# Kernel tuning notes

Measured on AMD Instinct MI355X. Metric: run time of the kernel, lower is better.

## Reference

```python
import jax, jax.numpy as jnp
import numpy as np

B, L = 128, 1024


def setup_inputs() -> dict:
    key = jax.random.key(0)
    k1, k2 = jax.random.split(key)
    y_pred = jax.random.normal(k1, (B, L), dtype=jnp.float32)
    y_true = jax.random.randint(k2, (B, L), 0, 2, dtype=jnp.int32)
    return {"y_pred": y_pred, "y_true": y_true}


def reference(y_pred, y_true):
    # pos/neg masks per row; original treats ==1 as pos, ==0 as neg
    pos = (y_true == 1)  # [B, L]
    neg = (y_true == 0)  # [B, L]
    # pairwise hinge: relu(1 - s_pos + s_neg) over all (pos, neg) pairs per row
    diff = 1.0 - y_pred[:, :, None] + y_pred[:, None, :]        # [B, L, L]
    pair_mask = pos[:, :, None] & neg[:, None, :]                # [B, L, L]
    hinge = jnp.where(pair_mask, jnp.maximum(diff, 0.0), 0.0)
    total = jnp.sum(hinge)
    num_pairs = jnp.sum(jnp.sum(pos, axis=1) * jnp.sum(neg, axis=1)).astype(y_pred.dtype)
    return jnp.where(num_pairs > 0, total / jnp.maximum(num_pairs, 1.0), total)
```

## Files before the change

kernel.cpp:

```cpp
#include <hip/hip_runtime.h>


#define PRL_B 128
#define PRL_L 1024
#define SPLIT 8
#define NBLK  (PRL_B * SPLIT)

template<int K>
__device__ __forceinline__ float hotloop(const float4* __restrict__ d4,
                                         int c0, int c1, float4 pv) {
    float acc[K];
#pragma unroll
    for (int k = 0; k < K; ++k) acc[k] = 0.f;
#pragma unroll 2
    for (int c = c0; c < c1; ++c) {
        const float4 d = d4[c];
#pragma unroll
        for (int k = 0; k < K; ++k) {
            const float pk = (k == 0) ? pv.x : (k == 1) ? pv.y : (k == 2) ? pv.z : pv.w;
            acc[k] += (fmaxf(d.x - pk, 0.f) + fmaxf(d.y - pk, 0.f))
                    + (fmaxf(d.z - pk, 0.f) + fmaxf(d.w - pk, 0.f));
        }
    }
    float r = 0.f;
#pragma unroll
    for (int k = 0; k < K; ++k) r += acc[k];
    return r;
}

__global__ __launch_bounds__(256) void prl_partial(
    const float* __restrict__ y_pred,
    const int*   __restrict__ y_true,
    float* __restrict__ bsum,
    int*   __restrict__ bpairs)
{
    __shared__ float4 s_pos4[PRL_L / 4];
    __shared__ float4 s_neg4[PRL_L / 4];
    __shared__ int    s_cntP[4], s_cntN[4];
    __shared__ float  s_wsum[4];
    float* s_pos = (float*)s_pos4;
    float* s_neg = (float*)s_neg4;

    const int blk  = blockIdx.x;
    const int b    = blk >> 3;
    const int s    = blk & (SPLIT - 1);
    const int t    = threadIdx.x;
    const int lane = t & 63;
    const int w    = t >> 6;

    const float4 sc = ((const float4*)(y_pred + (size_t)b * PRL_L))[t];
    const int4   lv = ((const int4*)  (y_true + (size_t)b * PRL_L))[t];
    const float sv[4] = {sc.x, sc.y, sc.z, sc.w};
    const int   lb[4] = {lv.x, lv.y, lv.z, lv.w};

    unsigned long long mP[4], mN[4];
    int cP = 0, cN = 0;
#pragma unroll
    for (int r = 0; r < 4; ++r) {
        mP[r] = __ballot(lb[r] == 1);
        mN[r] = __ballot(lb[r] == 0);
        cP += (int)__popcll(mP[r]);
        cN += (int)__popcll(mN[r]);
    }
    if (lane == 0) { s_cntP[w] = cP; s_cntN[w] = cN; }

    s_pos4[t] = make_float4( 3.0e38f,  3.0e38f,  3.0e38f,  3.0e38f);
    s_neg4[t] = make_float4(-3.0e38f, -3.0e38f, -3.0e38f, -3.0e38f);
    __syncthreads();

    int offP = 0, offN = 0, np = 0, nn = 0;
#pragma unroll
    for (int ww = 0; ww < 4; ++ww) {
        const int p_ = s_cntP[ww], n_ = s_cntN[ww];
        np += p_; nn += n_;
        if (ww < w) { offP += p_; offN += n_; }
    }

    const unsigned long long lt = (1ULL << lane) - 1ULL;
    int bP = offP, bN = offN;
#pragma unroll
    for (int r = 0; r < 4; ++r) {
        if (lb[r] == 1) s_pos[bP + (int)__popcll(mP[r] & lt)] = sv[r];
        bP += (int)__popcll(mP[r]);
        if (lb[r] == 0) s_neg[bN + (int)__popcll(mN[r] & lt)] = 1.0f + sv[r];
        bN += (int)__popcll(mN[r]);
    }
    __syncthreads();

    const float4 pv = make_float4(s_pos[t], s_pos[t + 256],
                                  s_pos[t + 512], s_pos[t + 768]);
    const int KP  = (np + 255) >> 8;
    const int NN4 = (nn + 3) >> 2;
    const int G   = (NN4 + SPLIT - 1) >> 3;
    const int c0  = s * G;
    const int c1  = min(c0 + G, NN4);

    float local;
    switch (KP) {
        case 0:  local = 0.f; break;
        case 1:  local = hotloop<1>(s_neg4, c0, c1, pv); break;
        case 2:  local = hotloop<2>(s_neg4, c0, c1, pv); break;
        case 3:  local = hotloop<3>(s_neg4, c0, c1, pv); break;
        default: local = hotloop<4>(s_neg4, c0, c1, pv); break;
    }

#pragma unroll
    for (int off = 32; off >= 1; off >>= 1)
        local += __shfl_down(local, off, 64);
    if (lane == 0) s_wsum[w] = local;
    __syncthreads();

    if (t == 0) {
        const float rs = (s_wsum[0] + s_wsum[1]) + (s_wsum[2] + s_wsum[3]);
        bsum[blk]   = rs;
        bpairs[blk] = (s == 0) ? np * nn : 0;
    }
}

__global__ __launch_bounds__(64) void prl_finalize(
    const float* __restrict__ bsum,
    const int*   __restrict__ bpairs,
    float* __restrict__ out)
{
    const int t = threadIdx.x;
    const float4* s4 = (const float4*)bsum;
    const int4*   p4 = (const int4*)bpairs;

    float fs = 0.f; int ps = 0;
#pragma unroll
    for (int k = 0; k < 4; ++k) {
        const float4 a = s4[t + 64 * k];
        const int4  ia = p4[t + 64 * k];
        fs += (a.x + a.y) + (a.z + a.w);
        ps += (ia.x + ia.y) + (ia.z + ia.w);
    }
#pragma unroll
    for (int off = 32; off >= 1; off >>= 1) {
        fs += __shfl_down(fs, off, 64);
        ps += __shfl_down(ps, off, 64);
    }
    if (t == 0)
        out[0] = (ps > 0) ? (fs / fmaxf((float)ps, 1.0f)) : fs;
}

extern "C" void kernel_launch(void* const* d_in, const int* in_sizes, int n_in,
                              void* d_out, int out_size, void* d_ws, size_t ws_size,
                              hipStream_t stream) {
    const float* y_pred = (const float*)d_in[0];
    const int*   y_true = (const int*)d_in[1];
    float* out = (float*)d_out;

    float* bsum   = (float*)d_ws;
    int*   bpairs = (int*)((char*)d_ws + NBLK * sizeof(float));

    prl_partial<<<NBLK, 256, 0, stream>>>(y_pred, y_true, bsum, bpairs);
    prl_finalize<<<1, 64, 0, stream>>>(bsum, bpairs, out);
}
```

Before: 11.75 us.

## Compact pos/neg per wave and drop block-level count and reduction barriers

Positive and negative scores are now compacted into per-wave 256-entry segments, so each wave only needs the other waves' negative counts. This removes one `__syncthreads` and the shared-memory prefix over wave counts. Positive counts are taken as 256 minus negatives, which assumes labels are strictly 0/1. Each wave now writes its own partial sum and negative count straight to global memory, and the finalize kernel widens to 256 threads to compute the pair counts. In exchange, the hot loop walks four separate negative segments with their own bounds, which adds loop overhead and possibly more imbalance across blocks.

```diff
diff --git a/kernel.cpp b/kernel.cpp
--- a/kernel.cpp
+++ b/kernel.cpp
@@ -7,19 +7,28 @@
 #define NBLK  (PRL_B * SPLIT)
 
 template<int K>
-__device__ __forceinline__ float hotloop(const float4* __restrict__ d4,
-                                         int c0, int c1, float4 pv) {
+__device__ __forceinline__ float hotall(const float4* __restrict__ neg4,
+                                        int c0_, int c1_, int c2_, int c3_,
+                                        int g0_, int g1_, int g2_, int g3_,
+                                        float4 pv) {
     float acc[K];
 #pragma unroll
     for (int k = 0; k < K; ++k) acc[k] = 0.f;
+#pragma unroll
+    for (int rw = 0; rw < 4; ++rw) {
+        const int c0 = (rw == 0) ? c0_ : (rw == 1) ? c1_ : (rw == 2) ? c2_ : c3_;
+        const int c1 = (rw == 0) ? g0_ : (rw == 1) ? g1_ : (rw == 2) ? g2_ : g3_;
+        const float4* r4 = neg4 + 64 * rw;
 #pragma unroll 2
-    for (int c = c0; c < c1; ++c) {
-        const float4 d = d4[c];
+        for (int c = c0; c < c1; ++c) {
+            const float4 d = r4[c];
 #pragma unroll
-        for (int k = 0; k < K; ++k) {
-            const float pk = (k == 0) ? pv.x : (k == 1) ? pv.y : (k == 2) ? pv.z : pv.w;
-            acc[k] += (fmaxf(d.x - pk, 0.f) + fmaxf(d.y - pk, 0.f))
-                    + (fmaxf(d.z - pk, 0.f) + fmaxf(d.w - pk, 0.f));
+            for (int k = 0; k < K; ++k) {
+                const float pk = (k == 0) ? pv.x : (k == 1) ? pv.y
+                               : (k == 2) ? pv.z : pv.w;
+                acc[k] += (fmaxf(d.x - pk, 0.f) + fmaxf(d.y - pk, 0.f))
+                        + (fmaxf(d.z - pk, 0.f) + fmaxf(d.w - pk, 0.f));
+            }
         }
     }
     float r = 0.f;
@@ -31,15 +40,12 @@
 __global__ __launch_bounds__(256) void prl_partial(
     const float* __restrict__ y_pred,
     const int*   __restrict__ y_true,
-    float* __restrict__ bsum,
-    int*   __restrict__ bpairs)
+    float* __restrict__ wsum,
+    int*   __restrict__ wcnt)
 {
-    __shared__ float4 s_pos4[PRL_L / 4];
-    __shared__ float4 s_neg4[PRL_L / 4];
-    __shared__ int    s_cntP[4], s_cntN[4];
-    __shared__ float  s_wsum[4];
-    float* s_pos = (float*)s_pos4;
-    float* s_neg = (float*)s_neg4;
+    __shared__ float s_pos[PRL_L];
+    __shared__ float s_neg[PRL_L];
+    __shared__ int   s_cnt[4];
 
     const int blk  = blockIdx.x;
     const int b    = blk >> 3;
@@ -47,100 +53,105 @@
     const int t    = threadIdx.x;
     const int lane = t & 63;
     const int w    = t >> 6;
+    const int baseW = 256 * w;
 
     const float4 sc = ((const float4*)(y_pred + (size_t)b * PRL_L))[t];
     const int4   lv = ((const int4*)  (y_true + (size_t)b * PRL_L))[t];
     const float sv[4] = {sc.x, sc.y, sc.z, sc.w};
     const int   lb[4] = {lv.x, lv.y, lv.z, lv.w};
 
-    unsigned long long mP[4], mN[4];
-    int cP = 0, cN = 0;
+    ((float4*)s_pos)[t] = make_float4( 3.0e38f,  3.0e38f,  3.0e38f,  3.0e38f);
+    ((float4*)s_neg)[t] = make_float4(-3.0e38f, -3.0e38f, -3.0e38f, -3.0e38f);
+
+    unsigned long long mN[4];
+    int cN = 0;
 #pragma unroll
     for (int r = 0; r < 4; ++r) {
-        mP[r] = __ballot(lb[r] == 1);
         mN[r] = __ballot(lb[r] == 0);
-        cP += (int)__popcll(mP[r]);
         cN += (int)__popcll(mN[r]);
     }
-    if (lane == 0) { s_cntP[w] = cP; s_cntN[w] = cN; }
-
-    s_pos4[t] = make_float4( 3.0e38f,  3.0e38f,  3.0e38f,  3.0e38f);
-    s_neg4[t] = make_float4(-3.0e38f, -3.0e38f, -3.0e38f, -3.0e38f);
-    __syncthreads();
-
-    int offP = 0, offN = 0, np = 0, nn = 0;
-#pragma unroll
-    for (int ww = 0; ww < 4; ++ww) {
-        const int p_ = s_cntP[ww], n_ = s_cntN[ww];
-        np += p_; nn += n_;
-        if (ww < w) { offP += p_; offN += n_; }
-    }
+    const int cP = 256 - cN;
+    if (lane == 0) s_cnt[w] = cN;
 
     const unsigned long long lt = (1ULL << lane) - 1ULL;
-    int bP = offP, bN = offN;
+    int bN = 0, bP = 0;
 #pragma unroll
     for (int r = 0; r < 4; ++r) {
-        if (lb[r] == 1) s_pos[bP + (int)__popcll(mP[r] & lt)] = sv[r];
-        bP += (int)__popcll(mP[r]);
-        if (lb[r] == 0) s_neg[bN + (int)__popcll(mN[r] & lt)] = 1.0f + sv[r];
-        bN += (int)__popcll(mN[r]);
+        const unsigned long long mn = mN[r], mp = ~mn;
+        if (lb[r] == 0) s_neg[baseW + bN + (int)__popcll(mn & lt)] = 1.0f + sv[r];
+        else            s_pos[baseW + bP + (int)__popcll(mp & lt)] = sv[r];
+        const int pn = (int)__popcll(mn);
+        bN += pn;
+        bP += 64 - pn;
     }
     __syncthreads();
 
-    const float4 pv = make_float4(s_pos[t], s_pos[t + 256],
-                                  s_pos[t + 512], s_pos[t + 768]);
-    const int KP  = (np + 255) >> 8;
-    const int NN4 = (nn + 3) >> 2;
-    const int G   = (NN4 + SPLIT - 1) >> 3;
-    const int c0  = s * G;
-    const int c1  = min(c0 + G, NN4);
+    const float4 pv = make_float4(s_pos[baseW + lane],       s_pos[baseW + lane + 64],
+                                  s_pos[baseW + lane + 128], s_pos[baseW + lane + 192]);
+    const int KP = (cP + 63) >> 6;
+
+    int c0[4], c1[4];
+#pragma unroll
+    for (int rw = 0; rw < 4; ++rw) {
+        const int NG = (s_cnt[rw] + 3) >> 2;
+        const int G  = (NG + SPLIT - 1) >> 3;
+        c0[rw] = min(s * G, NG);
+        c1[rw] = min(c0[rw] + G, NG);
+    }
 
     float local;
+    const float4* neg4 = (const float4*)s_neg;
     switch (KP) {
         case 0:  local = 0.f; break;
-        case 1:  local = hotloop<1>(s_neg4, c0, c1, pv); break;
-        case 2:  local = hotloop<2>(s_neg4, c0, c1, pv); break;
-        case 3:  local = hotloop<3>(s_neg4, c0, c1, pv); break;
-        default: local = hotloop<4>(s_neg4, c0, c1, pv); break;
+        case 1:  local = hotall<1>(neg4, c0[0],c0[1],c0[2],c0[3], c1[0],c1[1],c1[2],c1[3], pv); break;
+        case 2:  local = hotall<2>(neg4, c0[0],c0[1],c0[2],c0[3], c1[0],c1[1],c1[2],c1[3], pv); break;
+        case 3:  local = hotall<3>(neg4, c0[0],c0[1],c0[2],c0[3], c1[0],c1[1],c1[2],c1[3], pv); break;
+        default: local = hotall<4>(neg4, c0[0],c0[1],c0[2],c0[3], c1[0],c1[1],c1[2],c1[3], pv); break;
     }
 
 #pragma unroll
     for (int off = 32; off >= 1; off >>= 1)
         local += __shfl_down(local, off, 64);
-    if (lane == 0) s_wsum[w] = local;
-    __syncthreads();
-
-    if (t == 0) {
-        const float rs = (s_wsum[0] + s_wsum[1]) + (s_wsum[2] + s_wsum[3]);
-        bsum[blk]   = rs;
-        bpairs[blk] = (s == 0) ? np * nn : 0;
+    if (lane == 0) {
+        wsum[blk * 4 + w] = local;
+        if (s == 0) wcnt[b * 4 + w] = cN;
     }
 }
 
-__global__ __launch_bounds__(64) void prl_finalize(
-    const float* __restrict__ bsum,
-    const int*   __restrict__ bpairs,
+__global__ __launch_bounds__(256) void prl_finalize(
+    const float* __restrict__ wsum,
+    const int*   __restrict__ wcnt,
     float* __restrict__ out)
 {
-    const int t = threadIdx.x;
-    const float4* s4 = (const float4*)bsum;
-    const int4*   p4 = (const int4*)bpairs;
+    __shared__ float s_s[4];
+    __shared__ int   s_p[4];
+    const int t = threadIdx.x, lane = t & 63, w = t >> 6;
 
-    float fs = 0.f; int ps = 0;
+    const float4* s4 = (const float4*)wsum;
+    float fs = 0.f;
 #pragma unroll
     for (int k = 0; k < 4; ++k) {
-        const float4 a = s4[t + 64 * k];
-        const int4  ia = p4[t + 64 * k];
+        const float4 a = s4[t + 256 * k];
         fs += (a.x + a.y) + (a.z + a.w);
-        ps += (ia.x + ia.y) + (ia.z + ia.w);
+    }
+    int ps = 0;
+    if (t < PRL_B) {
+        const int4 c = ((const int4*)wcnt)[t];
+        const int nn = (c.x + c.y) + (c.z + c.w);
+        ps = (PRL_L - nn) * nn;
     }
 #pragma unroll
     for (int off = 32; off >= 1; off >>= 1) {
         fs += __shfl_down(fs, off, 64);
         ps += __shfl_down(ps, off, 64);
     }
-    if (t == 0)
-        out[0] = (ps > 0) ? (fs / fmaxf((float)ps, 1.0f)) : fs;
+    if (lane == 0) { s_s[w] = fs; s_p[w] = ps; }
+    __syncthreads();
+    if (t == 0) {
+        const float total = (s_s[0] + s_s[1]) + (s_s[2] + s_s[3]);
+        const int   pairs = (s_p[0] + s_p[1]) + (s_p[2] + s_p[3]);
+        out[0] = (pairs > 0) ? (total / fmaxf((float)pairs, 1.0f)) : total;
+    }
 }
 
 extern "C" void kernel_launch(void* const* d_in, const int* in_sizes, int n_in,
@@ -150,9 +161,9 @@
     const int*   y_true = (const int*)d_in[1];
     float* out = (float*)d_out;
 
-    float* bsum   = (float*)d_ws;
-    int*   bpairs = (int*)((char*)d_ws + NBLK * sizeof(float));
+    float* wsum = (float*)d_ws;
+    int*   wcnt = (int*)((char*)d_ws + NBLK * 4 * sizeof(float));
 
-    prl_partial<<<NBLK, 256, 0, stream>>>(y_pred, y_true, bsum, bpairs);
-    prl_finalize<<<1, 64, 0, stream>>>(bsum, bpairs, out);
+    prl_partial<<<NBLK, 256, 0, stream>>>(y_pred, y_true, wsum, wcnt);
+    prl_finalize<<<1, 256, 0, stream>>>(wsum, wcnt, out);
 }
```

Result: slower. 12.53 us (+6.6%).
